# Performance work log

Measured on AMD Instinct MI355X. Metric: run time of the kernel, lower is better.

The kernel has to match this reference:

```python
import jax, jax.numpy as jnp
import numpy as np

N_NODES = 50000


def _gcn_norm(edge_index, n):
    # improved=True: self-loops with weight 2.0, sym normalization
    src, dst = edge_index[0], edge_index[1]
    loop = jnp.arange(n, dtype=src.dtype)
    src_f = jnp.concatenate([src, loop])
    dst_f = jnp.concatenate([dst, loop])
    ew = jnp.concatenate([jnp.ones(src.shape[0], jnp.float32),
                          jnp.full((n,), 2.0, jnp.float32)])
    deg = jax.ops.segment_sum(ew, dst_f, num_segments=n)
    dinv = jnp.where(deg > 0, jax.lax.rsqrt(deg), 0.0)
    norm = dinv[src_f] * ew * dinv[dst_f]
    return src_f, dst_f, norm


def _gcn_conv(x, W, b, src_f, dst_f, norm, n):
    h = x @ W  # [N, C_out]
    msg = h[src_f] * norm[:, None]  # gather + scale, [E+N, C_out]
    out = jax.ops.segment_sum(msg, dst_f, num_segments=n)  # scatter-add
    return out + b


def setup_inputs() -> dict:
    key = jax.random.key(0)
    ks = jax.random.split(key, 12)
    n, f_in, h, labels, e = N_NODES, 256, 128, 128, 800000
    s = 1.0 / np.sqrt(f_in)
    sh = 1.0 / np.sqrt(h)
    return {
        "x": jax.random.normal(ks[0], (n, f_in), jnp.float32),
        "edge_index": jax.random.randint(ks[1], (2, e), 0, n, jnp.int64),
        "W1": jax.random.uniform(ks[2], (f_in, h), jnp.float32, -s, s),
        "b1": jnp.zeros((h,), jnp.float32),
        "W2": jax.random.uniform(ks[3], (h, h), jnp.float32, -sh, sh),
        "b2": jnp.zeros((h,), jnp.float32),
        "We": jax.random.uniform(ks[4], (h, h), jnp.float32, -sh, sh),
        "be": jnp.zeros((h,), jnp.float32),
        "Wf": jax.random.uniform(ks[5], (h, labels), jnp.float32, -sh, sh),
        "bf": jax.random.uniform(ks[6], (labels,), jnp.float32, -sh, sh),
    }


def reference(x, edge_index, W1, b1, W2, b2, We, be, Wf, bf):
    n = x.shape[0]
    src_f, dst_f, norm = _gcn_norm(edge_index, n)
    h = jax.nn.relu(_gcn_conv(x, W1, b1, src_f, dst_f, norm, n))
    h = jax.nn.relu(_gcn_conv(h, W2, b2, src_f, dst_f, norm, n))
    h = _gcn_conv(h, We, be, src_f, dst_f, norm, n)
    return jax.nn.sigmoid(h @ Wf + bf)
```

## Files before the change

kernel.cpp:

```cpp
#include <hip/hip_runtime.h>
#include <stdint.h>

static constexpr int NN  = 50000;
static constexpr int EE  = 800000;
static constexpr int FIN = 256;
static constexpr int HID = 128;
static constexpr int SCAN_NB = (NN + 1023) / 1024;

typedef __attribute__((ext_vector_type(8))) short  short8;
typedef __attribute__((ext_vector_type(8))) __bf16 bf16x8;
typedef __attribute__((ext_vector_type(4))) float  f32x4;
typedef uint16_t u16;

__device__ __forceinline__ u16 f2bf(float f) {
  union { float f; uint32_t u; } v; v.f = f;
  return (u16)((v.u + 0x7fffu + ((v.u >> 16) & 1u)) >> 16);
}
__device__ __forceinline__ float bf2f(u16 b) {
  union { uint32_t u; float f; } v; v.u = ((uint32_t)b) << 16;
  return v.f;
}
__device__ __forceinline__ float bflo(uint32_t u) {
  union { uint32_t u; float f; } v; v.u = u << 16; return v.f;
}
__device__ __forceinline__ float bfhi(uint32_t u) {
  union { uint32_t u; float f; } v; v.u = u & 0xffff0000u; return v.f;
}

__global__ void k_zero(int* p, int n) {
  int i = blockIdx.x * 256 + threadIdx.x;
  if (i < n) p[i] = 0;
}

__global__ void k_count(const int* __restrict__ dst, int* __restrict__ cnt, int e) {
  int i = blockIdx.x * 256 + threadIdx.x;
  if (i < e) atomicAdd(&cnt[dst[i]], 1);
}

__global__ __launch_bounds__(1024) void k_scan1(const int* __restrict__ cnt, int* __restrict__ incl,
                                                int* __restrict__ bsum, int n) {
  __shared__ int buf[1024];
  int tid = threadIdx.x;
  int i = blockIdx.x * 1024 + tid;
  int v = (i < n) ? cnt[i] : 0;
  buf[tid] = v;
  __syncthreads();
  for (int ofs = 1; ofs < 1024; ofs <<= 1) {
    int t = (tid >= ofs) ? buf[tid - ofs] : 0;
    __syncthreads();
    buf[tid] += t;
    __syncthreads();
  }
  if (i < n) incl[i] = buf[tid];
  if (tid == 1023) bsum[blockIdx.x] = buf[tid];
}

__global__ __launch_bounds__(1024) void k_scan3(const int* __restrict__ cnt, const int* __restrict__ incl,
                                                const int* __restrict__ bsum, int* __restrict__ off,
                                                int* __restrict__ cur, float* __restrict__ dinv, int n) {
  __shared__ int boff_s;
  int tid = threadIdx.x;
  if (tid < 64) {
    int v = (tid < (int)blockIdx.x) ? bsum[tid] : 0;
    for (int o = 32; o > 0; o >>= 1) v += __shfl_down(v, o);
    if (tid == 0) boff_s = v;
  }
  __syncthreads();
  int boff = boff_s;
  int i = blockIdx.x * 1024 + tid;
  if (i < n) {
    int v = cnt[i];
    int ex = boff + incl[i] - v;
    off[i] = ex;
    cur[i] = ex;
    dinv[i] = rsqrtf((float)v + 2.0f);
  }
  if (i == n - 1) off[n] = boff + incl[i];
}

__global__ void k_fill(const int* __restrict__ src, const int* __restrict__ dst, int* __restrict__ cur,
                       const float* __restrict__ dinv, int2* __restrict__ edges, int e) {
  int i = blockIdx.x * 256 + threadIdx.x;
  if (i < e) {
    int s = src[i], d = dst[i];
    int pos = atomicAdd(&cur[d], 1);
    edges[pos] = make_int2(s, __float_as_int(dinv[s] * dinv[d]));
  }
}

__global__ void k_wconv_all(const float* __restrict__ W1, const float* __restrict__ W2,
                            const float* __restrict__ We, const float* __restrict__ Wf,
                            u16* __restrict__ T1, u16* __restrict__ T2,
                            u16* __restrict__ T3, u16* __restrict__ T4) {
  int i = blockIdx.x * 256 + threadIdx.x;
  const float* W; u16* o;
  if (i < 32768)      { W = W1; o = T1; }
  else if (i < 49152) { W = W2; o = T2; i -= 32768; }
  else if (i < 65536) { W = We; o = T3; i -= 49152; }
  else                { W = Wf; o = T4; i -= 65536; }
  int k = i >> 7, c = i & 127;
  o[(size_t)((k >> 5) * 128 + c) * 32 + (k & 31)] = f2bf(W[i]);
}

template<int AFLOAT, int EPI>
__global__ __launch_bounds__(256) void k_gemm(const float* __restrict__ Af, const u16* __restrict__ Ah,
                                              const u16* __restrict__ Wt, const float* __restrict__ bias,
                                              u16* __restrict__ gout, float* __restrict__ fout,
                                              int M, int K) {
  __shared__ u16 Ash[64 * 40];
  __shared__ u16 Bsh[128 * 40];
  const int tid  = threadIdx.x;
  const int lane = tid & 63;
  const int w    = tid >> 6;
  const int row0 = blockIdx.x * 64;
  f32x4 acc[8];
#pragma unroll
  for (int t = 0; t < 8; ++t) acc[t] = (f32x4){0.f, 0.f, 0.f, 0.f};

  const int nk = K >> 5;
  const int r = tid >> 2, kg = tid & 3;
  const int grow_a = row0 + r;
  for (int kb = 0; kb < nk; ++kb) {
    {
      int k0 = kb * 32 + kg * 8;
      alignas(16) u16 v[8];
      if (grow_a < M) {
        if (AFLOAT) {
          const float* p = Af + (size_t)grow_a * K + k0;
          float4 x0 = *(const float4*)(p);
          float4 x1 = *(const float4*)(p + 4);
          v[0] = f2bf(x0.x); v[1] = f2bf(x0.y); v[2] = f2bf(x0.z); v[3] = f2bf(x0.w);
          v[4] = f2bf(x1.x); v[5] = f2bf(x1.y); v[6] = f2bf(x1.z); v[7] = f2bf(x1.w);
        } else {
          *(uint4*)v = *(const uint4*)(Ah + (size_t)grow_a * K + k0);
        }
      } else {
#pragma unroll
        for (int i = 0; i < 8; ++i) v[i] = 0;
      }
      *(uint4*)&Ash[r * 40 + kg * 8] = *(const uint4*)v;
    }
    {
      const u16* wsrc = Wt + (size_t)kb * 4096;
#pragma unroll
      for (int j = 0; j < 2; ++j) {
        int chunk = tid * 2 + j;
        int rowb = chunk >> 2, kk = (chunk & 3) << 3;
        *(uint4*)&Bsh[rowb * 40 + kk] = *(const uint4*)(wsrc + chunk * 8);
      }
    }
    __syncthreads();
    {
      const int rl = lane & 15, kq = lane >> 4;
      short8 af = *(const short8*)&Ash[(w * 16 + rl) * 40 + kq * 8];
#pragma unroll
      for (int t = 0; t < 8; ++t) {
        short8 bf = *(const short8*)&Bsh[(t * 16 + rl) * 40 + kq * 8];
        acc[t] = __builtin_amdgcn_mfma_f32_16x16x32_bf16(
            __builtin_bit_cast(bf16x8, af), __builtin_bit_cast(bf16x8, bf), acc[t], 0, 0, 0);
      }
    }
    __syncthreads();
  }
  const int rl = lane & 15, rq = lane >> 4;
#pragma unroll
  for (int t = 0; t < 8; ++t) {
    int col = t * 16 + rl;
#pragma unroll
    for (int i = 0; i < 4; ++i) {
      int grow = row0 + w * 16 + rq * 4 + i;
      if (grow < M) {
        if (EPI == 0) {
          gout[(size_t)grow * HID + col] = f2bf(acc[t][i]);
        } else {
          float vv = acc[t][i] + bias[col];
          fout[(size_t)grow * HID + col] = 1.0f / (1.0f + __expf(-vv));
        }
      }
    }
  }
}

template<int RELU>
__global__ __launch_bounds__(256) void k_agg(const u16* __restrict__ h, u16* __restrict__ g,
                                             const float* __restrict__ bias, const float* __restrict__ dinv,
                                             const int* __restrict__ off, const int2* __restrict__ edges,
                                             int n) {
  int wave = blockIdx.x * 4 + (threadIdx.x >> 6);
  int lane = threadIdx.x & 63;
  if (wave >= n) return;
  const int d  = wave;
  const int gr = lane >> 4;
  const int t  = lane & 15;
  const int c  = t << 3;
  float a[8];
#pragma unroll
  for (int i = 0; i < 8; ++i) a[i] = 0.f;

  int j  = off[d] + gr;
  const int j1 = off[d + 1];
  for (; j + 4 < j1; j += 8) {
    int2 eA = edges[j], eB = edges[j + 4];
    uint4 vA = *(const uint4*)(h + (size_t)eA.x * HID + c);
    uint4 vB = *(const uint4*)(h + (size_t)eB.x * HID + c);
    float wA = __int_as_float(eA.y), wB = __int_as_float(eB.y);
    a[0] += wA * bflo(vA.x); a[1] += wA * bfhi(vA.x);
    a[2] += wA * bflo(vA.y); a[3] += wA * bfhi(vA.y);
    a[4] += wA * bflo(vA.z); a[5] += wA * bfhi(vA.z);
    a[6] += wA * bflo(vA.w); a[7] += wA * bfhi(vA.w);
    a[0] += wB * bflo(vB.x); a[1] += wB * bfhi(vB.x);
    a[2] += wB * bflo(vB.y); a[3] += wB * bfhi(vB.y);
    a[4] += wB * bflo(vB.z); a[5] += wB * bfhi(vB.z);
    a[6] += wB * bflo(vB.w); a[7] += wB * bfhi(vB.w);
  }
  for (; j < j1; j += 4) {
    int2 eA = edges[j];
    uint4 vA = *(const uint4*)(h + (size_t)eA.x * HID + c);
    float wA = __int_as_float(eA.y);
    a[0] += wA * bflo(vA.x); a[1] += wA * bfhi(vA.x);
    a[2] += wA * bflo(vA.y); a[3] += wA * bfhi(vA.y);
    a[4] += wA * bflo(vA.z); a[5] += wA * bfhi(vA.z);
    a[6] += wA * bflo(vA.w); a[7] += wA * bfhi(vA.w);
  }
#pragma unroll
  for (int i = 0; i < 8; ++i) {
    a[i] += __shfl_xor(a[i], 16);
    a[i] += __shfl_xor(a[i], 32);
  }
  float di = dinv[d];
  float sl = 2.0f * di * di;
  uint4 sv = *(const uint4*)(h + (size_t)d * HID + c);
  const float4 bv0 = *(const float4*)(bias + c);
  const float4 bv1 = *(const float4*)(bias + c + 4);
  a[0] += sl * bflo(sv.x) + bv0.x; a[1] += sl * bfhi(sv.x) + bv0.y;
  a[2] += sl * bflo(sv.y) + bv0.z; a[3] += sl * bfhi(sv.y) + bv0.w;
  a[4] += sl * bflo(sv.z) + bv1.x; a[5] += sl * bfhi(sv.z) + bv1.y;
  a[6] += sl * bflo(sv.w) + bv1.z; a[7] += sl * bfhi(sv.w) + bv1.w;
  if (RELU) {
#pragma unroll
    for (int i = 0; i < 8; ++i) a[i] = fmaxf(a[i], 0.f);
  }
  if (gr == 0) {
    uint4 o;
    o.x = (uint32_t)f2bf(a[0]) | ((uint32_t)f2bf(a[1]) << 16);
    o.y = (uint32_t)f2bf(a[2]) | ((uint32_t)f2bf(a[3]) << 16);
    o.z = (uint32_t)f2bf(a[4]) | ((uint32_t)f2bf(a[5]) << 16);
    o.w = (uint32_t)f2bf(a[6]) | ((uint32_t)f2bf(a[7]) << 16);
    *(uint4*)(g + (size_t)d * HID + c) = o;
  }
}

extern "C" void kernel_launch(void* const* d_in, const int* in_sizes, int n_in,
                              void* d_out, int out_size, void* d_ws, size_t ws_size,
                              hipStream_t stream) {
  const float* x   = (const float*)d_in[0];
  const int*   ei  = (const int*)d_in[1];
  const float* W1  = (const float*)d_in[2];
  const float* b1  = (const float*)d_in[3];
  const float* W2  = (const float*)d_in[4];
  const float* b2  = (const float*)d_in[5];
  const float* We  = (const float*)d_in[6];
  const float* be  = (const float*)d_in[7];
  const float* Wf  = (const float*)d_in[8];
  const float* bfv = (const float*)d_in[9];
  float* out = (float*)d_out;

  const int* src = ei;
  const int* dst = ei + EE;

  char* p = (char*)d_ws;
  auto take = [&](size_t bytes) { char* r = p; p += (bytes + 255) & ~(size_t)255; return r; };
  int*   cnt   = (int*)take((size_t)NN * 4);
  int*   incl  = (int*)take((size_t)NN * 4);
  int*   bsum  = (int*)take((size_t)SCAN_NB * 4);
  int*   off   = (int*)take((size_t)(NN + 1) * 4);
  int*   cur   = (int*)take((size_t)NN * 4);
  float* dinv  = (float*)take((size_t)NN * 4);
  int2*  edges = (int2*)take((size_t)EE * 8);
  u16*   hA    = (u16*)take((size_t)NN * HID * 2);
  u16*   hB    = (u16*)take((size_t)NN * HID * 2);
  u16*   Wt1   = (u16*)take((size_t)FIN * HID * 2);
  u16*   Wt2   = (u16*)take((size_t)HID * HID * 2);
  u16*   Wt3   = (u16*)take((size_t)HID * HID * 2);
  u16*   Wt4   = (u16*)take((size_t)HID * HID * 2);

  k_zero<<<(NN + 255) / 256, 256, 0, stream>>>(cnt, NN);
  k_count<<<(EE + 255) / 256, 256, 0, stream>>>(dst, cnt, EE);
  k_scan1<<<SCAN_NB, 1024, 0, stream>>>(cnt, incl, bsum, NN);
  k_scan3<<<SCAN_NB, 1024, 0, stream>>>(cnt, incl, bsum, off, cur, dinv, NN);
  k_fill<<<(EE + 255) / 256, 256, 0, stream>>>(src, dst, cur, dinv, edges, EE);

  k_wconv_all<<<(81920 + 255) / 256, 256, 0, stream>>>(W1, W2, We, Wf, Wt1, Wt2, Wt3, Wt4);

  const int gemm_grid = (NN + 63) / 64;
  const int agg_grid  = (NN + 3) / 4;

  k_gemm<1, 0><<<gemm_grid, 256, 0, stream>>>(x, nullptr, Wt1, nullptr, hA, nullptr, NN, FIN);
  k_agg<1><<<agg_grid, 256, 0, stream>>>(hA, hB, b1, dinv, off, edges, NN);
  k_gemm<0, 0><<<gemm_grid, 256, 0, stream>>>(nullptr, hB, Wt2, nullptr, hA, nullptr, NN, HID);
  k_agg<1><<<agg_grid, 256, 0, stream>>>(hA, hB, b2, dinv, off, edges, NN);
  k_gemm<0, 0><<<gemm_grid, 256, 0, stream>>>(nullptr, hB, Wt3, nullptr, hA, nullptr, NN, HID);
  k_agg<0><<<agg_grid, 256, 0, stream>>>(hA, hB, be, dinv, off, edges, NN);
  k_gemm<0, 1><<<gemm_grid, 256, 0, stream>>>(nullptr, hB, Wt4, bfv, nullptr, out, NN, HID);
}
```

Before: 346.5 us.

## Build CSR via two-level bucket sort with shared-memory atomics

Replaces the global per-node atomic counting, multi-block scan and atomic fill with a two-pass bucket sort. Edges are first binned into 256-node buckets using block-local histograms, then each bucket block counts, scans and fills its nodes with shared-memory atomics. The hB activation buffer is reused as scratch for the bucketed edges. The aim is to cut global atomic contention and scattered writes in CSR construction, at the cost of extra passes over the edge list and more kernel launches.

```diff
diff --git a/kernel.cpp b/kernel.cpp
--- a/kernel.cpp
+++ b/kernel.cpp
@@ -5,7 +5,10 @@
 static constexpr int EE  = 800000;
 static constexpr int FIN = 256;
 static constexpr int HID = 128;
-static constexpr int SCAN_NB = (NN + 1023) / 1024;
+static constexpr int SZ_LOG = 8;
+static constexpr int NBUCK  = (NN + 255) >> SZ_LOG;
+static constexpr int CH     = 2048;
+static constexpr int NCBLK  = (EE + CH - 1) / CH;
 
 typedef __attribute__((ext_vector_type(8))) short  short8;
 typedef __attribute__((ext_vector_type(8))) __bf16 bf16x8;
@@ -16,10 +19,6 @@
   union { float f; uint32_t u; } v; v.f = f;
   return (u16)((v.u + 0x7fffu + ((v.u >> 16) & 1u)) >> 16);
 }
-__device__ __forceinline__ float bf2f(u16 b) {
-  union { uint32_t u; float f; } v; v.u = ((uint32_t)b) << 16;
-  return v.f;
-}
 __device__ __forceinline__ float bflo(uint32_t u) {
   union { uint32_t u; float f; } v; v.u = u << 16; return v.f;
 }
@@ -32,59 +31,109 @@
   if (i < n) p[i] = 0;
 }
 
-__global__ void k_count(const int* __restrict__ dst, int* __restrict__ cnt, int e) {
-  int i = blockIdx.x * 256 + threadIdx.x;
-  if (i < e) atomicAdd(&cnt[dst[i]], 1);
-}
-
-__global__ __launch_bounds__(1024) void k_scan1(const int* __restrict__ cnt, int* __restrict__ incl,
-                                                int* __restrict__ bsum, int n) {
-  __shared__ int buf[1024];
+__global__ __launch_bounds__(256) void k_bhist(const int* __restrict__ dst, int* __restrict__ bcnt, int e) {
+  __shared__ int lc[NBUCK];
   int tid = threadIdx.x;
-  int i = blockIdx.x * 1024 + tid;
-  int v = (i < n) ? cnt[i] : 0;
+  for (int i = tid; i < NBUCK; i += 256) lc[i] = 0;
+  __syncthreads();
+  int base = blockIdx.x * CH;
+#pragma unroll
+  for (int j = 0; j < 8; ++j) {
+    int i = base + j * 256 + tid;
+    if (i < e) atomicAdd(&lc[dst[i] >> SZ_LOG], 1);
+  }
+  __syncthreads();
+  for (int i = tid; i < NBUCK; i += 256) if (lc[i]) atomicAdd(&bcnt[i], lc[i]);
+}
+
+__global__ __launch_bounds__(256) void k_bscan(const int* __restrict__ bcnt, int* __restrict__ boff,
+                                               int* __restrict__ bcur, int* __restrict__ off) {
+  __shared__ int buf[256];
+  int tid = threadIdx.x;
+  int v = (tid < NBUCK) ? bcnt[tid] : 0;
   buf[tid] = v;
   __syncthreads();
-  for (int ofs = 1; ofs < 1024; ofs <<= 1) {
-    int t = (tid >= ofs) ? buf[tid - ofs] : 0;
+  for (int o = 1; o < 256; o <<= 1) {
+    int t = (tid >= o) ? buf[tid - o] : 0;
     __syncthreads();
     buf[tid] += t;
     __syncthreads();
   }
-  if (i < n) incl[i] = buf[tid];
-  if (tid == 1023) bsum[blockIdx.x] = buf[tid];
-}
-
-__global__ __launch_bounds__(1024) void k_scan3(const int* __restrict__ cnt, const int* __restrict__ incl,
-                                                const int* __restrict__ bsum, int* __restrict__ off,
-                                                int* __restrict__ cur, float* __restrict__ dinv, int n) {
-  __shared__ int boff_s;
+  int ex = buf[tid] - v;
+  if (tid < NBUCK) { boff[tid] = ex; bcur[tid] = ex; }
+  if (tid == NBUCK - 1) boff[NBUCK] = ex + v;
+  if (tid == 0) off[NN] = EE;
+}
+
+__global__ __launch_bounds__(256) void k_bscatter(const int* __restrict__ src, const int* __restrict__ dst,
+                                                  int* __restrict__ bcur, int2* __restrict__ ebuck, int e) {
+  __shared__ int lc[NBUCK];
+  __shared__ int lb[NBUCK];
   int tid = threadIdx.x;
-  if (tid < 64) {
-    int v = (tid < (int)blockIdx.x) ? bsum[tid] : 0;
-    for (int o = 32; o > 0; o >>= 1) v += __shfl_down(v, o);
-    if (tid == 0) boff_s = v;
-  }
-  __syncthreads();
-  int boff = boff_s;
-  int i = blockIdx.x * 1024 + tid;
-  if (i < n) {
-    int v = cnt[i];
-    int ex = boff + incl[i] - v;
-    off[i] = ex;
-    cur[i] = ex;
-    dinv[i] = rsqrtf((float)v + 2.0f);
-  }
-  if (i == n - 1) off[n] = boff + incl[i];
-}
-
-__global__ void k_fill(const int* __restrict__ src, const int* __restrict__ dst, int* __restrict__ cur,
-                       const float* __restrict__ dinv, int2* __restrict__ edges, int e) {
-  int i = blockIdx.x * 256 + threadIdx.x;
-  if (i < e) {
-    int s = src[i], d = dst[i];
-    int pos = atomicAdd(&cur[d], 1);
-    edges[pos] = make_int2(s, __float_as_int(dinv[s] * dinv[d]));
+  for (int i = tid; i < NBUCK; i += 256) lc[i] = 0;
+  __syncthreads();
+  int base = blockIdx.x * CH;
+  int sj[8], dj[8], rj[8];
+#pragma unroll
+  for (int j = 0; j < 8; ++j) {
+    int i = base + j * 256 + tid;
+    if (i < e) {
+      sj[j] = src[i]; dj[j] = dst[i];
+      rj[j] = atomicAdd(&lc[dj[j] >> SZ_LOG], 1);
+    }
+  }
+  __syncthreads();
+  for (int i = tid; i < NBUCK; i += 256) { int c = lc[i]; if (c) lb[i] = atomicAdd(&bcur[i], c); }
+  __syncthreads();
+#pragma unroll
+  for (int j = 0; j < 8; ++j) {
+    int i = base + j * 256 + tid;
+    if (i < e) ebuck[lb[dj[j] >> SZ_LOG] + rj[j]] = make_int2(sj[j], dj[j]);
+  }
+}
+
+__global__ __launch_bounds__(256) void k_ncount(const int2* __restrict__ ebuck, const int* __restrict__ boff,
+                                                int* __restrict__ off, float* __restrict__ dinv) {
+  __shared__ int nc[256];
+  __shared__ int sc[256];
+  int b = blockIdx.x, tid = threadIdx.x;
+  nc[tid] = 0;
+  __syncthreads();
+  int j0 = boff[b], j1 = boff[b + 1];
+  for (int j = j0 + tid; j < j1; j += 256) atomicAdd(&nc[ebuck[j].y & 255], 1);
+  __syncthreads();
+  int v = nc[tid];
+  sc[tid] = v;
+  __syncthreads();
+  for (int o = 1; o < 256; o <<= 1) {
+    int t = (tid >= o) ? sc[tid - o] : 0;
+    __syncthreads();
+    sc[tid] += t;
+    __syncthreads();
+  }
+  int node = (b << SZ_LOG) + tid;
+  if (node < NN) {
+    off[node]  = j0 + sc[tid] - v;
+    dinv[node] = rsqrtf((float)v + 2.0f);
+  }
+}
+
+__global__ __launch_bounds__(256) void k_fill2(const int2* __restrict__ ebuck, const int* __restrict__ boff,
+                                               const int* __restrict__ off, const float* __restrict__ dinv,
+                                               int2* __restrict__ edges) {
+  __shared__ int   lcur[256];
+  __shared__ float ldv[256];
+  int b = blockIdx.x, tid = threadIdx.x;
+  int node = (b << SZ_LOG) + tid;
+  lcur[tid] = (node < NN) ? off[node]  : 0;
+  ldv[tid]  = (node < NN) ? dinv[node] : 0.f;
+  __syncthreads();
+  int j0 = boff[b], j1 = boff[b + 1];
+  for (int j = j0 + tid; j < j1; j += 256) {
+    int2 e = ebuck[j];
+    int loc = e.y & 255;
+    int pos = atomicAdd(&lcur[loc], 1);
+    edges[pos] = make_int2(e.x, __float_as_int(dinv[e.x] * ldv[loc]));
   }
 }
 
@@ -270,11 +319,10 @@
 
   char* p = (char*)d_ws;
   auto take = [&](size_t bytes) { char* r = p; p += (bytes + 255) & ~(size_t)255; return r; };
-  int*   cnt   = (int*)take((size_t)NN * 4);
-  int*   incl  = (int*)take((size_t)NN * 4);
-  int*   bsum  = (int*)take((size_t)SCAN_NB * 4);
+  int*   bcnt  = (int*)take((size_t)NBUCK * 4);
+  int*   boff  = (int*)take((size_t)(NBUCK + 1) * 4);
+  int*   bcur  = (int*)take((size_t)NBUCK * 4);
   int*   off   = (int*)take((size_t)(NN + 1) * 4);
-  int*   cur   = (int*)take((size_t)NN * 4);
   float* dinv  = (float*)take((size_t)NN * 4);
   int2*  edges = (int2*)take((size_t)EE * 8);
   u16*   hA    = (u16*)take((size_t)NN * HID * 2);
@@ -283,12 +331,14 @@
   u16*   Wt2   = (u16*)take((size_t)HID * HID * 2);
   u16*   Wt3   = (u16*)take((size_t)HID * HID * 2);
   u16*   Wt4   = (u16*)take((size_t)HID * HID * 2);
-
-  k_zero<<<(NN + 255) / 256, 256, 0, stream>>>(cnt, NN);
-  k_count<<<(EE + 255) / 256, 256, 0, stream>>>(dst, cnt, EE);
-  k_scan1<<<SCAN_NB, 1024, 0, stream>>>(cnt, incl, bsum, NN);
-  k_scan3<<<SCAN_NB, 1024, 0, stream>>>(cnt, incl, bsum, off, cur, dinv, NN);
-  k_fill<<<(EE + 255) / 256, 256, 0, stream>>>(src, dst, cur, dinv, edges, EE);
+  int2*  ebuck = (int2*)hB;
+
+  k_zero<<<1, 256, 0, stream>>>(bcnt, NBUCK);
+  k_bhist<<<NCBLK, 256, 0, stream>>>(dst, bcnt, EE);
+  k_bscan<<<1, 256, 0, stream>>>(bcnt, boff, bcur, off);
+  k_bscatter<<<NCBLK, 256, 0, stream>>>(src, dst, bcur, ebuck, EE);
+  k_ncount<<<NBUCK, 256, 0, stream>>>(ebuck, boff, off, dinv);
+  k_fill2<<<NBUCK, 256, 0, stream>>>(ebuck, boff, off, dinv, edges);
 
   k_wconv_all<<<(81920 + 255) / 256, 256, 0, stream>>>(W1, W2, We, Wf, Wt1, Wt2, Wt3, Wt4);
 
```

Result: faster. 304.0 us (-12.3%).
